# Kernel optimization log

Measured on AMD Instinct MI355X. Metric: run time of the kernel, lower is better.

The kernel has to match this reference:

```python
import jax, jax.numpy as jnp
import numpy as np

N_NODES = 100000
N_EDGES = 1600000
N_GRAPHS = 128
K_HOPS = 3  # TAGConv default K
HIDDEN = 128
IN_FEAT = 4
NUM_CLASSES = 2


def setup_inputs() -> dict:
    key = jax.random.key(0)
    ks = jax.random.split(key, 10)
    x = jax.random.normal(ks[0], (N_NODES, IN_FEAT), dtype=jnp.float32)
    W1 = jax.random.normal(ks[1], (K_HOPS + 1, IN_FEAT, HIDDEN), dtype=jnp.float32) * 0.1
    b1 = jax.random.normal(ks[2], (HIDDEN,), dtype=jnp.float32) * 0.1
    W2 = jax.random.normal(ks[3], (K_HOPS + 1, HIDDEN, HIDDEN), dtype=jnp.float32) * 0.1
    b2 = jax.random.normal(ks[4], (HIDDEN,), dtype=jnp.float32) * 0.1
    Wlin = jax.random.normal(ks[5], (HIDDEN, NUM_CLASSES), dtype=jnp.float32) * 0.1
    blin = jax.random.normal(ks[6], (NUM_CLASSES,), dtype=jnp.float32) * 0.1
    edge_index = jax.random.randint(ks[7], (2, N_EDGES), 0, N_NODES, dtype=jnp.int32)
    batch = jnp.sort(jax.random.randint(ks[8], (N_NODES,), 0, N_GRAPHS, dtype=jnp.int32))
    return {"x": x, "W1": W1, "b1": b1, "W2": W2, "b2": b2,
            "Wlin": Wlin, "blin": blin, "edge_index": edge_index, "batch": batch}


def _gcn_norm(edge_index, num_nodes):
    # symmetric normalization, no self-loops (TAGConv: add_self_loops=False)
    row, col = edge_index[0], edge_index[1]
    ones = jnp.ones((edge_index.shape[1],), dtype=jnp.float32)
    deg = jax.ops.segment_sum(ones, col, num_segments=num_nodes)
    dinv = jnp.where(deg > 0, jax.lax.rsqrt(jnp.maximum(deg, 1.0)), 0.0)
    return dinv[row] * dinv[col]  # [E]


def _tagconv(x, row, col, norm, W, b):
    # out = sum_k (A_norm^k x) @ W[k] + b
    out = x @ W[0]
    h = x
    for k in range(1, W.shape[0]):
        h = jax.ops.segment_sum(h[row] * norm[:, None], col, num_segments=x.shape[0])
        out = out + h @ W[k]
    return out + b


def reference(x, W1, b1, W2, b2, Wlin, blin, edge_index, batch):
    row, col = edge_index[0], edge_index[1]
    norm = _gcn_norm(edge_index, x.shape[0])
    h = jax.nn.relu(_tagconv(x, row, col, norm, W1, b1))
    h = jax.nn.relu(_tagconv(h, row, col, norm, W2, b2))
    # global mean pool over graphs
    sums = jax.ops.segment_sum(h, batch, num_segments=N_GRAPHS)
    cnts = jax.ops.segment_sum(jnp.ones((h.shape[0],), dtype=h.dtype), batch, num_segments=N_GRAPHS)
    pooled = sums / jnp.maximum(cnts, 1.0)[:, None]
    # dropout is identity in eval mode
    logits = pooled @ Wlin + blin
    return jax.nn.softmax(logits, axis=-1)
```

## Files before the change

### kernel.cpp

```cpp
#include <hip/hip_runtime.h>

#define NNODES 100000
#define NEDGES 1600000
#define NGRAPHS 128
#define HID 128
#define NBKT 782
#define NPAD  (NBKT * 128)
#define CHUNK 8192
#define NCHB ((NEDGES + CHUNK - 1) / CHUNK)
#define MAXB 3072

typedef unsigned short ushort_t;
typedef unsigned int uint_t;
typedef __attribute__((ext_vector_type(8))) short short8;
typedef __attribute__((ext_vector_type(4))) float floatx4;

__device__ __forceinline__ float bf2f(ushort_t u) {
    return __uint_as_float(((unsigned)u) << 16);
}
__device__ __forceinline__ ushort_t f2bf(float f) {
    unsigned u = __float_as_uint(f);
    return (ushort_t)((u + 0x7fffu + ((u >> 16) & 1u)) >> 16);
}

__global__ void hist_k(const int* __restrict__ col, int* __restrict__ bcnt) {
    __shared__ int l[NBKT];
    for (int i = threadIdx.x; i < NBKT; i += 256) l[i] = 0;
    __syncthreads();
    int base = blockIdx.x * CHUNK;
    int lim = base + CHUNK < NEDGES ? base + CHUNK : NEDGES;
    for (int e = base + threadIdx.x; e < lim; e += 256)
        atomicAdd(&l[col[e] >> 7], 1);
    __syncthreads();
    for (int i = threadIdx.x; i < NBKT; i += 256)
        if (l[i]) atomicAdd(&bcnt[i], l[i]);
}

__global__ void bscan_k(const int* __restrict__ bcnt, int* __restrict__ bbase,
                        int* __restrict__ gc) {
    __shared__ int l[1024];
    int t = threadIdx.x;
    int v0 = (t < NBKT) ? bcnt[t] : 0;
    l[t] = v0;
    __syncthreads();
    for (int d = 1; d < 1024; d <<= 1) {
        int v = (t >= d) ? l[t - d] : 0;
        __syncthreads();
        l[t] += v;
        __syncthreads();
    }
    if (t < NBKT) { int ex = l[t] - v0; bbase[t] = ex; gc[t] = ex; }
    if (t == 0) bbase[NBKT] = NEDGES;
}

__global__ void bfill_k(const int* __restrict__ row, const int* __restrict__ col,
                        int* __restrict__ gc, uint_t* __restrict__ entry) {
    __shared__ int lcnt[NBKT], lbase[NBKT];
    for (int i = threadIdx.x; i < NBKT; i += 256) lcnt[i] = 0;
    __syncthreads();
    int base = blockIdx.x * CHUNK;
    int lim = base + CHUNK < NEDGES ? base + CHUNK : NEDGES;
    for (int e = base + threadIdx.x; e < lim; e += 256)
        atomicAdd(&lcnt[col[e] >> 7], 1);
    __syncthreads();
    for (int i = threadIdx.x; i < NBKT; i += 256) {
        int c = lcnt[i];
        lbase[i] = c ? atomicAdd(&gc[i], c) : 0;
        lcnt[i] = 0;
    }
    __syncthreads();
    for (int e = base + threadIdx.x; e < lim; e += 256) {
        int c = col[e];
        int b = c >> 7;
        int pos = lbase[b] + atomicAdd(&lcnt[b], 1);
        entry[pos] = (uint_t)row[e] | ((uint_t)(c & 127) << 17);
    }
}

__global__ void sortb_k(const uint_t* __restrict__ entry, const int* __restrict__ bbase,
                        int* __restrict__ csr_src, int* __restrict__ degi,
                        int* __restrict__ off, int* __restrict__ perm) {
    __shared__ uint_t ents[MAXB];
    __shared__ uint_t sorted[MAXB];
    __shared__ int ncnt[128], nsc[128], nfill[128];
    __shared__ int dcnt[64], dbase_s[64], dfill[64];
    int b = blockIdx.x;
    int base = bbase[b];
    int cnt = bbase[b + 1] - base;
    if (cnt > MAXB) cnt = MAXB;
    int t = threadIdx.x;
    if (t < 128) { ncnt[t] = 0; nfill[t] = 0; }
    if (t >= 128 && t < 192) { dcnt[t - 128] = 0; dfill[t - 128] = 0; }
    __syncthreads();
    for (int i = t; i < cnt; i += 256) {
        uint_t v = entry[base + i];
        ents[i] = v;
        atomicAdd(&ncnt[v >> 17], 1);
    }
    __syncthreads();
    if (t < 128) nsc[t] = ncnt[t];
    __syncthreads();
    for (int d = 1; d < 128; d <<= 1) {
        int v = (t >= d && t < 128) ? nsc[t - d] : 0;
        __syncthreads();
        if (t < 128) nsc[t] += v;
        __syncthreads();
    }
    int mydeg = 0;
    if (t < 128) {
        int n = b * 128 + t;
        if (n < NNODES) { degi[n] = ncnt[t]; off[n] = base + nsc[t]; }
        nsc[t] -= ncnt[t];
        mydeg = ncnt[t] > 63 ? 63 : ncnt[t];
        atomicAdd(&dcnt[mydeg], 1);
    }
    __syncthreads();
    for (int i = t; i < cnt; i += 256) {
        uint_t v = ents[i];
        int dl = v >> 17;
        int pos = nsc[dl] + atomicAdd(&nfill[dl], 1);
        sorted[pos] = v & 0x1FFFFu;
    }
    if (t == 0) {
        int run = 0;
        for (int i = 0; i < 64; i++) { dbase_s[i] = run; run += dcnt[i]; }
    }
    __syncthreads();
    if (t < 128) {
        int pos = dbase_s[mydeg] + atomicAdd(&dfill[mydeg], 1);
        perm[b * 128 + pos] = b * 128 + t;
    }
    for (int i = t; i < cnt; i += 256) csr_src[base + i] = (int)sorted[i];
}

__global__ void misc_k(const int* __restrict__ degi, float* __restrict__ dinv,
                       const float* __restrict__ W2, ushort_t* __restrict__ Wt,
                       const int* __restrict__ batch,
                       int* __restrict__ first, int* __restrict__ last) {
    int i = blockIdx.x * 256 + threadIdx.x;
    if (i < NNODES) {
        int d = degi[i];
        dinv[i] = (d > 0) ? rsqrtf((float)d) : 0.0f;
        int g = batch[i];
        if (i == 0 || batch[i - 1] != g) first[g] = i;
        if (i == NNODES - 1 || batch[i + 1] != g) last[g] = i;
    }
    if (i < 512 * 128) {
        int j = i >> 9, k = i & 511;
        Wt[i] = f2bf(W2[k * 128 + j]);
    }
}

__global__ void gprop4(const int* __restrict__ off, const int* __restrict__ csr_src,
                       const float* __restrict__ dinv, const int* __restrict__ perm,
                       const float* __restrict__ hin, float* __restrict__ hout) {
    int i = blockIdx.x * 256 + threadIdx.x;
    if (i >= NPAD) return;
    int n = perm[i];
    if (n >= NNODES) return;
    int k = n ? off[n - 1] : 0;
    int end = off[n];
    float dn = dinv[n];
    float4 acc = {0.f, 0.f, 0.f, 0.f};
    for (; k + 3 < end; k += 4) {
        int s0 = csr_src[k], s1 = csr_src[k + 1], s2 = csr_src[k + 2], s3 = csr_src[k + 3];
        float w0 = dinv[s0] * dn, w1 = dinv[s1] * dn, w2 = dinv[s2] * dn, w3 = dinv[s3] * dn;
        float4 v0 = *(const float4*)(hin + s0 * 4);
        float4 v1 = *(const float4*)(hin + s1 * 4);
        float4 v2 = *(const float4*)(hin + s2 * 4);
        float4 v3 = *(const float4*)(hin + s3 * 4);
        acc.x += w0 * v0.x + w1 * v1.x + w2 * v2.x + w3 * v3.x;
        acc.y += w0 * v0.y + w1 * v1.y + w2 * v2.y + w3 * v3.y;
        acc.z += w0 * v0.z + w1 * v1.z + w2 * v2.z + w3 * v3.z;
        acc.w += w0 * v0.w + w1 * v1.w + w2 * v2.w + w3 * v3.w;
    }
    for (; k < end; k++) {
        int s = csr_src[k];
        float w = dinv[s] * dn;
        float4 v = *(const float4*)(hin + s * 4);
        acc.x += w * v.x; acc.y += w * v.y; acc.z += w * v.z; acc.w += w * v.w;
    }
    *(float4*)(hout + n * 4) = acc;
}

__device__ __forceinline__ void acc8(float* a, float wgt, uint4 v) {
    a[0] += wgt * __uint_as_float(v.x << 16);
    a[1] += wgt * __uint_as_float(v.x & 0xffff0000u);
    a[2] += wgt * __uint_as_float(v.y << 16);
    a[3] += wgt * __uint_as_float(v.y & 0xffff0000u);
    a[4] += wgt * __uint_as_float(v.z << 16);
    a[5] += wgt * __uint_as_float(v.z & 0xffff0000u);
    a[6] += wgt * __uint_as_float(v.w << 16);
    a[7] += wgt * __uint_as_float(v.w & 0xffff0000u);
}

__global__ void gprop128(const int* __restrict__ off, const int* __restrict__ csr_src,
                         const float* __restrict__ dinv, const int* __restrict__ perm,
                         const ushort_t* __restrict__ hin, ushort_t* __restrict__ hout) {
    int t = blockIdx.x * 256 + threadIdx.x;
    int i = t >> 4, lane = t & 15;
    if (i >= NPAD) return;
    int n = perm[i];
    if (n >= NNODES) return;
    int k = n ? off[n - 1] : 0;
    int end = off[n];
    float dn = dinv[n];
    int fo = lane * 8;
    float a[8] = {0.f, 0.f, 0.f, 0.f, 0.f, 0.f, 0.f, 0.f};
    for (; k + 3 < end; k += 4) {
        int s0 = csr_src[k], s1 = csr_src[k + 1], s2 = csr_src[k + 2], s3 = csr_src[k + 3];
        float w0 = dinv[s0] * dn, w1 = dinv[s1] * dn, w2 = dinv[s2] * dn, w3 = dinv[s3] * dn;
        uint4 v0 = *(const uint4*)(hin + s0 * HID + fo);
        uint4 v1 = *(const uint4*)(hin + s1 * HID + fo);
        uint4 v2 = *(const uint4*)(hin + s2 * HID + fo);
        uint4 v3 = *(const uint4*)(hin + s3 * HID + fo);
        acc8(a, w0, v0); acc8(a, w1, v1); acc8(a, w2, v2); acc8(a, w3, v3);
    }
    for (; k < end; k++) {
        int s = csr_src[k];
        float w = dinv[s] * dn;
        uint4 v = *(const uint4*)(hin + s * HID + fo);
        acc8(a, w, v);
    }
    uint4 o;
    o.x = (unsigned)f2bf(a[0]) | ((unsigned)f2bf(a[1]) << 16);
    o.y = (unsigned)f2bf(a[2]) | ((unsigned)f2bf(a[3]) << 16);
    o.z = (unsigned)f2bf(a[4]) | ((unsigned)f2bf(a[5]) << 16);
    o.w = (unsigned)f2bf(a[6]) | ((unsigned)f2bf(a[7]) << 16);
    *(uint4*)(hout + n * HID + fo) = o;
}

__global__ void combine1(const float* __restrict__ x, const float* __restrict__ h1,
                         const float* __restrict__ h2, const float* __restrict__ h3,
                         const float* __restrict__ W1, const float* __restrict__ b1,
                         ushort_t* __restrict__ P0) {
    __shared__ float hs[4][16];
    int n0 = blockIdx.x * 4;
    int j = threadIdx.x;
    if (j < 64) {
        int n = j >> 4, v = j & 15, k = v >> 2, i = v & 3;
        const float* src = (k == 0) ? x : (k == 1) ? h1 : (k == 2) ? h2 : h3;
        hs[n][v] = src[(n0 + n) * 4 + i];
    }
    __syncthreads();
    float w[16];
#pragma unroll
    for (int v = 0; v < 16; v++) w[v] = W1[v * 128 + j];
    float bb = b1[j];
#pragma unroll
    for (int n = 0; n < 4; n++) {
        float acc = bb;
#pragma unroll
        for (int v = 0; v < 16; v++) acc += hs[n][v] * w[v];
        P0[(n0 + n) * 128 + j] = f2bf(fmaxf(acc, 0.0f));
    }
}

__global__ __launch_bounds__(256) void gemm4p(
    const ushort_t* __restrict__ P0, const ushort_t* __restrict__ P1,
    const ushort_t* __restrict__ P2, const ushort_t* __restrict__ P3,
    const ushort_t* __restrict__ Wt, const float* __restrict__ b2,
    const int* __restrict__ batch, float* __restrict__ sums) {
    __shared__ ushort_t Bs[32768];
    int tid = threadIdx.x;
    int w = tid >> 6, lane = tid & 63;
    int r16 = lane & 15, kg = lane >> 4;
    int tb = blockIdx.x * 128 + w * 32;
    bool active = (tb < NNODES);
    floatx4 acc[2][8];
#pragma unroll
    for (int s = 0; s < 2; s++)
#pragma unroll
        for (int n = 0; n < 8; n++) acc[s][n] = (floatx4){0.f, 0.f, 0.f, 0.f};
    const ushort_t* Ps[4] = {P0, P1, P2, P3};
    for (int stage = 0; stage < 2; stage++) {
        __syncthreads();
#pragma unroll
        for (int i = 0; i < 16; i++) {
            int idx = i * 256 + tid;
            int r = idx >> 5;
            int slot = idx & 31;
            int cb = (slot * 16) ^ ((r & 7) << 4);
            *(uint4*)((char*)Bs + r * 512 + cb) =
                *(const uint4*)(Wt + r * 512 + stage * 256 + slot * 8);
        }
        __syncthreads();
        if (active) {
#pragma unroll
            for (int hh = 0; hh < 2; hh++) {
                const ushort_t* P = Ps[stage * 2 + hh];
#pragma unroll
                for (int k0 = 0; k0 < 128; k0 += 32) {
                    int f = k0 + kg * 8;
                    short8 a0 = *(const short8*)(P + (tb + r16) * HID + f);
                    short8 a1 = *(const short8*)(P + (tb + 16 + r16) * HID + f);
#pragma unroll
                    for (int n = 0; n < 8; n++) {
                        int r = n * 16 + r16;
                        int cb = (hh * 256 + k0 * 2 + kg * 16) ^ ((r & 7) << 4);
                        short8 b = *(const short8*)((const char*)Bs + r * 512 + cb);
                        acc[0][n] = __builtin_amdgcn_mfma_f32_16x16x32_bf16(a0, b, acc[0][n], 0, 0, 0);
                        acc[1][n] = __builtin_amdgcn_mfma_f32_16x16x32_bf16(a1, b, acc[1][n], 0, 0, 0);
                    }
                }
            }
        }
    }
    if (!active) return;
    float bb[8];
#pragma unroll
    for (int n = 0; n < 8; n++) bb[n] = b2[n * 16 + r16];
    int g0 = batch[tb], g31 = batch[tb + 31];
    if (g0 == g31) {
#pragma unroll
        for (int n = 0; n < 8; n++) {
            float s = 0.0f;
#pragma unroll
            for (int st = 0; st < 2; st++)
#pragma unroll
                for (int r = 0; r < 4; r++) s += fmaxf(acc[st][n][r] + bb[n], 0.0f);
            s += __shfl_xor(s, 16);
            s += __shfl_xor(s, 32);
            if (kg == 0) atomicAdd(&sums[g0 * HID + n * 16 + r16], s);
        }
    } else {
#pragma unroll
        for (int st = 0; st < 2; st++)
#pragma unroll
            for (int r = 0; r < 4; r++) {
                int g = batch[tb + st * 16 + kg * 4 + r];
#pragma unroll
                for (int n = 0; n < 8; n++)
                    atomicAdd(&sums[g * HID + n * 16 + r16], fmaxf(acc[st][n][r] + bb[n], 0.0f));
            }
    }
}

__global__ void head_kernel(const float* __restrict__ sums, const int* __restrict__ first,
                            const int* __restrict__ last,
                            const float* __restrict__ Wlin, const float* __restrict__ blin,
                            float* __restrict__ out) {
    int g = threadIdx.x;
    if (g >= NGRAPHS) return;
    float cnt = (float)(last[g] - first[g] + 1);
    if (cnt < 1.0f) cnt = 1.0f;
    float l0 = blin[0], l1 = blin[1];
    for (int i = 0; i < HID; i++) {
        float p = sums[g * HID + i] / cnt;
        l0 += p * Wlin[i * 2 + 0];
        l1 += p * Wlin[i * 2 + 1];
    }
    float m = fmaxf(l0, l1);
    float e0 = __expf(l0 - m), e1 = __expf(l1 - m);
    float s = e0 + e1;
    out[g * 2 + 0] = e0 / s;
    out[g * 2 + 1] = e1 / s;
}

#define OFF_DINV  0
#define OFF_DEGI  (OFF_DINV + NPAD)
#define OFF_OFF   (OFF_DEGI + NPAD)
#define OFF_PERM  (OFF_OFF + NPAD)
#define OFF_SUMS  (OFF_PERM + NPAD)
#define OFF_FIRST (OFF_SUMS + NGRAPHS * HID)
#define OFF_LAST  (OFF_FIRST + NGRAPHS)
#define OFF_BCNT  (OFF_LAST + NGRAPHS)
#define ZERO_WORDS (NGRAPHS * HID + NGRAPHS + NGRAPHS + 800)
#define OFF_BBASE (OFF_BCNT + 800)
#define OFF_GC    (OFF_BBASE + 800)
#define OFF_ENT   (OFF_GC + 800)
#define OFF_SRC   (OFF_ENT + NEDGES)
#define OFF_P0    (OFF_SRC + NEDGES)
#define OFF_P1    (OFF_P0 + NNODES * HID / 2)
#define OFF_P2    (OFF_P1 + NNODES * HID / 2)
#define OFF_P3    (OFF_P2 + NNODES * HID / 2)
#define OFF_H1    (OFF_P3 + NNODES * HID / 2)
#define OFF_H2    (OFF_H1 + NNODES * 4)
#define OFF_H3    (OFF_H2 + NNODES * 4)
#define OFF_WT    (OFF_H3 + NNODES * 4)

extern "C" void kernel_launch(void* const* d_in, const int* in_sizes, int n_in,
                              void* d_out, int out_size, void* d_ws, size_t ws_size,
                              hipStream_t stream) {
    const float* x    = (const float*)d_in[0];
    const float* W1   = (const float*)d_in[1];
    const float* b1   = (const float*)d_in[2];
    const float* W2   = (const float*)d_in[3];
    const float* b2   = (const float*)d_in[4];
    const float* Wlin = (const float*)d_in[5];
    const float* blin = (const float*)d_in[6];
    const int* ei     = (const int*)d_in[7];
    const int* batch  = (const int*)d_in[8];
    float* out = (float*)d_out;

    const int* row = ei;
    const int* col = ei + NEDGES;

    float* ws = (float*)d_ws;
    float* dinv    = ws + OFF_DINV;
    int*   degi    = (int*)(ws + OFF_DEGI);
    int*   off     = (int*)(ws + OFF_OFF);
    int*   perm    = (int*)(ws + OFF_PERM);
    float* sums    = ws + OFF_SUMS;
    int*   first   = (int*)(ws + OFF_FIRST);
    int*   last    = (int*)(ws + OFF_LAST);
    int*   bcnt    = (int*)(ws + OFF_BCNT);
    int*   bbase   = (int*)(ws + OFF_BBASE);
    int*   gc      = (int*)(ws + OFF_GC);
    uint_t* ent    = (uint_t*)(ws + OFF_ENT);
    int*   csr_src = (int*)(ws + OFF_SRC);
    ushort_t* P0   = (ushort_t*)(ws + OFF_P0);
    ushort_t* P1   = (ushort_t*)(ws + OFF_P1);
    ushort_t* P2   = (ushort_t*)(ws + OFF_P2);
    ushort_t* P3   = (ushort_t*)(ws + OFF_P3);
    float* h1      = ws + OFF_H1;
    float* h2      = ws + OFF_H2;
    float* h3      = ws + OFF_H3;
    ushort_t* Wt   = (ushort_t*)(ws + OFF_WT);

    hipMemsetAsync(sums, 0, ZERO_WORDS * sizeof(float), stream);

    hist_k<<<NCHB, 256, 0, stream>>>(col, bcnt);
    bscan_k<<<1, 1024, 0, stream>>>(bcnt, bbase, gc);
    bfill_k<<<NCHB, 256, 0, stream>>>(row, col, gc, ent);
    sortb_k<<<NBKT, 256, 0, stream>>>(ent, bbase, csr_src, degi, off, perm);
    misc_k<<<(NPAD) / 256, 256, 0, stream>>>(degi, dinv, W2, Wt, batch, first, last);

    gprop4<<<NPAD / 256, 256, 0, stream>>>(off, csr_src, dinv, perm, x, h1);
    gprop4<<<NPAD / 256, 256, 0, stream>>>(off, csr_src, dinv, perm, h1, h2);
    gprop4<<<NPAD / 256, 256, 0, stream>>>(off, csr_src, dinv, perm, h2, h3);
    combine1<<<NNODES / 4, 128, 0, stream>>>(x, h1, h2, h3, W1, b1, P0);

    gprop128<<<NPAD * 16 / 256, 256, 0, stream>>>(off, csr_src, dinv, perm, P0, P1);
    gprop128<<<NPAD * 16 / 256, 256, 0, stream>>>(off, csr_src, dinv, perm, P1, P2);
    gprop128<<<NPAD * 16 / 256, 256, 0, stream>>>(off, csr_src, dinv, perm, P2, P3);

    gemm4p<<<(NNODES + 127) / 128, 256, 0, stream>>>(P0, P1, P2, P3, Wt, b2, batch, sums);

    head_kernel<<<1, 128, 0, stream>>>(sums, first, last, Wlin, blin, out);
}
```

Baseline: 402.3 us.

## Precompute per-edge CSR weights, drop degree-sorted permutation, unroll gather by eight

Adds a kernel that precomputes each edge's normalized weight into a CSR-aligned array (reusing the entry buffer). The six propagation kernels then read weights sequentially instead of doing a dependent random dinv lookup per edge. The per-bucket degree-sorting permutation is removed, so nodes are processed in natural order and the perm indirection disappears, at the cost of more warp divergence from uneven degrees. The 128-wide gather is unrolled to eight edges to keep more loads in flight.

```diff
diff --git a/kernel.cpp b/kernel.cpp
--- a/kernel.cpp
+++ b/kernel.cpp
@@ -79,18 +79,16 @@
 
 __global__ void sortb_k(const uint_t* __restrict__ entry, const int* __restrict__ bbase,
                         int* __restrict__ csr_src, int* __restrict__ degi,
-                        int* __restrict__ off, int* __restrict__ perm) {
+                        int* __restrict__ off) {
     __shared__ uint_t ents[MAXB];
     __shared__ uint_t sorted[MAXB];
     __shared__ int ncnt[128], nsc[128], nfill[128];
-    __shared__ int dcnt[64], dbase_s[64], dfill[64];
     int b = blockIdx.x;
     int base = bbase[b];
     int cnt = bbase[b + 1] - base;
     if (cnt > MAXB) cnt = MAXB;
     int t = threadIdx.x;
     if (t < 128) { ncnt[t] = 0; nfill[t] = 0; }
-    if (t >= 128 && t < 192) { dcnt[t - 128] = 0; dfill[t - 128] = 0; }
     __syncthreads();
     for (int i = t; i < cnt; i += 256) {
         uint_t v = entry[base + i];
@@ -106,13 +104,10 @@
         if (t < 128) nsc[t] += v;
         __syncthreads();
     }
-    int mydeg = 0;
     if (t < 128) {
         int n = b * 128 + t;
         if (n < NNODES) { degi[n] = ncnt[t]; off[n] = base + nsc[t]; }
         nsc[t] -= ncnt[t];
-        mydeg = ncnt[t] > 63 ? 63 : ncnt[t];
-        atomicAdd(&dcnt[mydeg], 1);
     }
     __syncthreads();
     for (int i = t; i < cnt; i += 256) {
@@ -121,15 +116,7 @@
         int pos = nsc[dl] + atomicAdd(&nfill[dl], 1);
         sorted[pos] = v & 0x1FFFFu;
     }
-    if (t == 0) {
-        int run = 0;
-        for (int i = 0; i < 64; i++) { dbase_s[i] = run; run += dcnt[i]; }
-    }
-    __syncthreads();
-    if (t < 128) {
-        int pos = dbase_s[mydeg] + atomicAdd(&dfill[mydeg], 1);
-        perm[b * 128 + pos] = b * 128 + t;
-    }
+    __syncthreads();
     for (int i = t; i < cnt; i += 256) csr_src[base + i] = (int)sorted[i];
 }
 
@@ -151,20 +138,27 @@
     }
 }
 
-__global__ void gprop4(const int* __restrict__ off, const int* __restrict__ csr_src,
-                       const float* __restrict__ dinv, const int* __restrict__ perm,
-                       const float* __restrict__ hin, float* __restrict__ hout) {
-    int i = blockIdx.x * 256 + threadIdx.x;
-    if (i >= NPAD) return;
-    int n = perm[i];
+__global__ void wfill_k(const int* __restrict__ off, const int* __restrict__ csr_src,
+                        const float* __restrict__ dinv, float* __restrict__ csr_w) {
+    int n = blockIdx.x * 256 + threadIdx.x;
     if (n >= NNODES) return;
     int k = n ? off[n - 1] : 0;
     int end = off[n];
     float dn = dinv[n];
+    for (; k < end; k++) csr_w[k] = dinv[csr_src[k]] * dn;
+}
+
+__global__ void gprop4(const int* __restrict__ off, const int* __restrict__ csr_src,
+                       const float* __restrict__ csr_w,
+                       const float* __restrict__ hin, float* __restrict__ hout) {
+    int n = blockIdx.x * 256 + threadIdx.x;
+    if (n >= NNODES) return;
+    int k = n ? off[n - 1] : 0;
+    int end = off[n];
     float4 acc = {0.f, 0.f, 0.f, 0.f};
     for (; k + 3 < end; k += 4) {
         int s0 = csr_src[k], s1 = csr_src[k + 1], s2 = csr_src[k + 2], s3 = csr_src[k + 3];
-        float w0 = dinv[s0] * dn, w1 = dinv[s1] * dn, w2 = dinv[s2] * dn, w3 = dinv[s3] * dn;
+        float w0 = csr_w[k], w1 = csr_w[k + 1], w2 = csr_w[k + 2], w3 = csr_w[k + 3];
         float4 v0 = *(const float4*)(hin + s0 * 4);
         float4 v1 = *(const float4*)(hin + s1 * 4);
         float4 v2 = *(const float4*)(hin + s2 * 4);
@@ -176,7 +170,7 @@
     }
     for (; k < end; k++) {
         int s = csr_src[k];
-        float w = dinv[s] * dn;
+        float w = csr_w[k];
         float4 v = *(const float4*)(hin + s * 4);
         acc.x += w * v.x; acc.y += w * v.y; acc.z += w * v.z; acc.w += w * v.w;
     }
@@ -195,32 +189,45 @@
 }
 
 __global__ void gprop128(const int* __restrict__ off, const int* __restrict__ csr_src,
-                         const float* __restrict__ dinv, const int* __restrict__ perm,
+                         const float* __restrict__ csr_w,
                          const ushort_t* __restrict__ hin, ushort_t* __restrict__ hout) {
     int t = blockIdx.x * 256 + threadIdx.x;
-    int i = t >> 4, lane = t & 15;
-    if (i >= NPAD) return;
-    int n = perm[i];
+    int n = t >> 4, lane = t & 15;
     if (n >= NNODES) return;
     int k = n ? off[n - 1] : 0;
     int end = off[n];
-    float dn = dinv[n];
     int fo = lane * 8;
     float a[8] = {0.f, 0.f, 0.f, 0.f, 0.f, 0.f, 0.f, 0.f};
-    for (; k + 3 < end; k += 4) {
+    for (; k + 7 < end; k += 8) {
         int s0 = csr_src[k], s1 = csr_src[k + 1], s2 = csr_src[k + 2], s3 = csr_src[k + 3];
-        float w0 = dinv[s0] * dn, w1 = dinv[s1] * dn, w2 = dinv[s2] * dn, w3 = dinv[s3] * dn;
+        int s4 = csr_src[k + 4], s5 = csr_src[k + 5], s6 = csr_src[k + 6], s7 = csr_src[k + 7];
         uint4 v0 = *(const uint4*)(hin + s0 * HID + fo);
         uint4 v1 = *(const uint4*)(hin + s1 * HID + fo);
         uint4 v2 = *(const uint4*)(hin + s2 * HID + fo);
         uint4 v3 = *(const uint4*)(hin + s3 * HID + fo);
-        acc8(a, w0, v0); acc8(a, w1, v1); acc8(a, w2, v2); acc8(a, w3, v3);
+        uint4 v4 = *(const uint4*)(hin + s4 * HID + fo);
+        uint4 v5 = *(const uint4*)(hin + s5 * HID + fo);
+        uint4 v6 = *(const uint4*)(hin + s6 * HID + fo);
+        uint4 v7 = *(const uint4*)(hin + s7 * HID + fo);
+        acc8(a, csr_w[k],     v0); acc8(a, csr_w[k + 1], v1);
+        acc8(a, csr_w[k + 2], v2); acc8(a, csr_w[k + 3], v3);
+        acc8(a, csr_w[k + 4], v4); acc8(a, csr_w[k + 5], v5);
+        acc8(a, csr_w[k + 6], v6); acc8(a, csr_w[k + 7], v7);
+    }
+    if (k + 3 < end) {
+        int s0 = csr_src[k], s1 = csr_src[k + 1], s2 = csr_src[k + 2], s3 = csr_src[k + 3];
+        uint4 v0 = *(const uint4*)(hin + s0 * HID + fo);
+        uint4 v1 = *(const uint4*)(hin + s1 * HID + fo);
+        uint4 v2 = *(const uint4*)(hin + s2 * HID + fo);
+        uint4 v3 = *(const uint4*)(hin + s3 * HID + fo);
+        acc8(a, csr_w[k],     v0); acc8(a, csr_w[k + 1], v1);
+        acc8(a, csr_w[k + 2], v2); acc8(a, csr_w[k + 3], v3);
+        k += 4;
     }
     for (; k < end; k++) {
         int s = csr_src[k];
-        float w = dinv[s] * dn;
         uint4 v = *(const uint4*)(hin + s * HID + fo);
-        acc8(a, w, v);
+        acc8(a, csr_w[k], v);
     }
     uint4 o;
     o.x = (unsigned)f2bf(a[0]) | ((unsigned)f2bf(a[1]) << 16);
@@ -360,8 +367,7 @@
 #define OFF_DINV  0
 #define OFF_DEGI  (OFF_DINV + NPAD)
 #define OFF_OFF   (OFF_DEGI + NPAD)
-#define OFF_PERM  (OFF_OFF + NPAD)
-#define OFF_SUMS  (OFF_PERM + NPAD)
+#define OFF_SUMS  (OFF_OFF + NPAD)
 #define OFF_FIRST (OFF_SUMS + NGRAPHS * HID)
 #define OFF_LAST  (OFF_FIRST + NGRAPHS)
 #define OFF_BCNT  (OFF_LAST + NGRAPHS)
@@ -400,7 +406,6 @@
     float* dinv    = ws + OFF_DINV;
     int*   degi    = (int*)(ws + OFF_DEGI);
     int*   off     = (int*)(ws + OFF_OFF);
-    int*   perm    = (int*)(ws + OFF_PERM);
     float* sums    = ws + OFF_SUMS;
     int*   first   = (int*)(ws + OFF_FIRST);
     int*   last    = (int*)(ws + OFF_LAST);
@@ -408,6 +413,7 @@
     int*   bbase   = (int*)(ws + OFF_BBASE);
     int*   gc      = (int*)(ws + OFF_GC);
     uint_t* ent    = (uint_t*)(ws + OFF_ENT);
+    float* csr_w   = ws + OFF_ENT;
     int*   csr_src = (int*)(ws + OFF_SRC);
     ushort_t* P0   = (ushort_t*)(ws + OFF_P0);
     ushort_t* P1   = (ushort_t*)(ws + OFF_P1);
@@ -423,17 +429,18 @@
     hist_k<<<NCHB, 256, 0, stream>>>(col, bcnt);
     bscan_k<<<1, 1024, 0, stream>>>(bcnt, bbase, gc);
     bfill_k<<<NCHB, 256, 0, stream>>>(row, col, gc, ent);
-    sortb_k<<<NBKT, 256, 0, stream>>>(ent, bbase, csr_src, degi, off, perm);
-    misc_k<<<(NPAD) / 256, 256, 0, stream>>>(degi, dinv, W2, Wt, batch, first, last);
-
-    gprop4<<<NPAD / 256, 256, 0, stream>>>(off, csr_src, dinv, perm, x, h1);
-    gprop4<<<NPAD / 256, 256, 0, stream>>>(off, csr_src, dinv, perm, h1, h2);
-    gprop4<<<NPAD / 256, 256, 0, stream>>>(off, csr_src, dinv, perm, h2, h3);
+    sortb_k<<<NBKT, 256, 0, stream>>>(ent, bbase, csr_src, degi, off);
+    misc_k<<<NPAD / 256, 256, 0, stream>>>(degi, dinv, W2, Wt, batch, first, last);
+    wfill_k<<<NPAD / 256, 256, 0, stream>>>(off, csr_src, dinv, csr_w);
+
+    gprop4<<<NPAD / 256, 256, 0, stream>>>(off, csr_src, csr_w, x, h1);
+    gprop4<<<NPAD / 256, 256, 0, stream>>>(off, csr_src, csr_w, h1, h2);
+    gprop4<<<NPAD / 256, 256, 0, stream>>>(off, csr_src, csr_w, h2, h3);
     combine1<<<NNODES / 4, 128, 0, stream>>>(x, h1, h2, h3, W1, b1, P0);
 
-    gprop128<<<NPAD * 16 / 256, 256, 0, stream>>>(off, csr_src, dinv, perm, P0, P1);
-    gprop128<<<NPAD * 16 / 256, 256, 0, stream>>>(off, csr_src, dinv, perm, P1, P2);
-    gprop128<<<NPAD * 16 / 256, 256, 0, stream>>>(off, csr_src, dinv, perm, P2, P3);
+    gprop128<<<NPAD * 16 / 256, 256, 0, stream>>>(off, csr_src, csr_w, P0, P1);
+    gprop128<<<NPAD * 16 / 256, 256, 0, stream>>>(off, csr_src, csr_w, P1, P2);
+    gprop128<<<NPAD * 16 / 256, 256, 0, stream>>>(off, csr_src, csr_w, P2, P3);
 
     gemm4p<<<(NNODES + 127) / 128, 256, 0, stream>>>(P0, P1, P2, P3, Wt, b2, batch, sums);
 
```

Measured after the change: 364.7 us. -9.3%, faster.
